# Performance work log

Measured on AMD Instinct MI355X. Metric: run time of the kernel, lower is better.

## Reference

```python
import jax, jax.numpy as jnp
import numpy as np

B, N, DIN, DOUT, H, DH, DC, NL, L = 8, 256, 64, 64, 8, 8, 64, 32, 2
SCALE = DH ** -0.5  # out_dim-per-head scaling used by both attention variants


def _ln(x, g, b):
    m = jnp.mean(x, -1, keepdims=True)
    v = jnp.mean((x - m) ** 2, -1, keepdims=True)
    return (x - m) * jax.lax.rsqrt(v + 1e-5) * g + b


def _cross_attn(x, ctx, mask_b, wq, wkv, wo, bo):
    # CrossAttentionLayer: standard softmax attention with clamp(-5,5)
    b, n, _ = x.shape
    m = ctx.shape[1]
    q = (x @ wq).reshape(b, n, H, DH).transpose(0, 2, 1, 3)
    k, v = jnp.split(ctx @ wkv, 2, axis=-1)
    k = k.reshape(b, m, H, DH).transpose(0, 2, 1, 3)
    v = v.reshape(b, m, H, DH).transpose(0, 2, 1, 3)
    sim = jnp.einsum('bhid,bhjd->bhij', q, k) * SCALE
    if mask_b is not None:
        sim = jnp.where(mask_b[:, None, None, :], sim, -jnp.finfo(sim.dtype).max)
    sim = jnp.clip(sim, -5.0, 5.0)
    attn = jax.nn.softmax(sim, axis=-1)
    out = jnp.einsum('bhij,bhjd->bhid', attn, v)
    out = out.transpose(0, 2, 1, 3).reshape(b, n, H * DH)
    return out @ wo + bo


def _mha_edge(p, e, k_RW, mask, wq, wk, we, wv):
    # GraphiT MultiHeadAttentionLayer with edge features + k_RW attention PE
    Q = (p @ wq).reshape(B, N, H, DH)
    K = (p @ wk).reshape(B, N, H, DH) * SCALE
    V = (p @ wv).reshape(B, N, H, DH).transpose(0, 2, 1, 3)  # [B,H,N,d]
    E = (e @ we).reshape(B, N, N, H, DH)
    scores = jnp.einsum('bihk,bjhk,bijhk->bhij', Q, K, E)
    scores = jnp.exp(scores - jnp.max(scores, axis=(-2, -1), keepdims=True))
    scores = scores * mask[:, None, :, None] * mask[:, None, None, :]
    scores = scores * k_RW
    denom = jnp.clip(jnp.sum(scores, -1, keepdims=True), 1e-6, None)
    out = jnp.einsum('bhij,bhjd->bhid', scores, V) / denom
    return out.transpose(0, 2, 1, 3).reshape(B, N, H * DH)


def setup_inputs() -> dict:
    key = jax.random.key(0)
    ks = jax.random.split(key, 32)
    rn = lambda k, s: jax.random.normal(k, s, dtype=jnp.float32)
    inp = {
        'h': rn(ks[0], (B, N, DIN)),
        'p': rn(ks[1], (B, N, DIN)),
        'e': rn(ks[2], (B, N, N, DIN)),
        'k_RW': jax.random.uniform(ks[3], (B, 1, N, N), dtype=jnp.float32),
        'queries': rn(ks[4], (B, NL, DC)),
        'mask': jnp.ones((B, N), dtype=jnp.float32),
        # attention_p (MultiHeadAttentionLayer) weights
        'wq_p': rn(ks[5], (DIN, H * DH)) * 0.05,
        'wk_p': rn(ks[6], (DIN, H * DH)) * 0.05,
        'we_p': rn(ks[7], (DIN, H * DH)) * 0.05,
        'wv_p': rn(ks[8], (DIN, H * DH)) * 0.05,
        'wo_p': rn(ks[9], (DOUT, DOUT)) * 0.05,
        # cross_attention_h (queries attend to nodes)
        'cq_wq': rn(ks[10], (DC, H * DH)) * 0.05,
        'cq_wkv': rn(ks[11], (DIN, 2 * H * DH)) * 0.05,
        'cq_wo': rn(ks[12], (H * DH, DC)) * 0.05,
        'cq_bo': jnp.zeros((DC,), dtype=jnp.float32),
        # L_cross latent self-attention layers (stacked)
        'sa_wq': rn(ks[13], (L, DC, H * DH)) * 0.05,
        'sa_wkv': rn(ks[14], (L, DC, 2 * H * DH)) * 0.05,
        'sa_wo': rn(ks[15], (L, H * DH, DC)) * 0.05,
        'sa_bo': jnp.zeros((L, DC), dtype=jnp.float32),
        # O_queries, norms, FFN
        'oq_w': rn(ks[16], (DC, DC)) * 0.05,
        'ln1_g': jnp.ones((DC,), dtype=jnp.float32),
        'ln1_b': jnp.zeros((DC,), dtype=jnp.float32),
        'ffn_w1': rn(ks[17], (DC, 2 * DC)) * 0.05,
        'ffn_w2': rn(ks[18], (2 * DC, DC)) * 0.05,
        'ln2_g': jnp.ones((DC,), dtype=jnp.float32),
        'ln2_b': jnp.zeros((DC,), dtype=jnp.float32),
    }
    return inp


def reference(h, p, e, k_RW, queries, mask,
              wq_p, wk_p, we_p, wv_p, wo_p,
              cq_wq, cq_wkv, cq_wo, cq_bo,
              sa_wq, sa_wkv, sa_wo, sa_bo,
              oq_w, ln1_g, ln1_b, ffn_w1, ffn_w2, ln2_g, ln2_b):
    # forward_p: update positional encoding via edge-modulated attention
    p_attn = _mha_edge(p, e, k_RW, mask, wq_p, wk_p, we_p, wv_p)
    p_new = p + jnp.tanh(p_attn @ wo_p)  # residual, no dropout (eval)
    # combine node features with updated PE (use_node_pe='sum')
    h_c = h + p_new
    mask_b = mask > 0.5
    # perceiver cross-attention: latents attend to nodes
    q = queries + _cross_attn(queries, h_c, mask_b, cq_wq, cq_wkv, cq_wo, cq_bo)
    # L_cross latent self-attention blocks with residual
    for i in range(L):
        q = q + _cross_attn(q, q, None, sa_wq[i], sa_wkv[i], sa_wo[i], sa_bo[i])
    # O_queries projection + layer norm
    q = _ln(q @ oq_w, ln1_g, ln1_b)
    # feed-forward block on queries
    ff = jax.nn.relu(q @ ffn_w1) @ ffn_w2
    q = _ln(q + ff, ln2_g, ln2_b)
    return q
```

## Files before the change

### kernel.cpp

```cpp
#include <hip/hip_runtime.h>
#include <hip/hip_bf16.h>
#include <math.h>

typedef __bf16 bf16x8 __attribute__((ext_vector_type(8)));
typedef float floatx4 __attribute__((ext_vector_type(4)));

#define ATT_SCALE 0.35355339059327373f

__device__ __forceinline__ __bf16 f2b(float x) { return (__bf16)x; }

__global__ void k_proj(const float* __restrict__ p, const float* __restrict__ quer,
                       const float* __restrict__ wq, const float* __restrict__ wk,
                       const float* __restrict__ wv, const float* __restrict__ cq_wq,
                       float* __restrict__ Q, float* __restrict__ Ks,
                       float* __restrict__ V, float* __restrict__ q1) {
  int blk = blockIdx.x, t = threadIdx.x;
  __shared__ float xr[64];
  if (blk < 2048) {
    xr[t] = p[blk * 64 + t];
    __syncthreads();
    float aq = 0.f, ak = 0.f, av = 0.f;
#pragma unroll
    for (int c = 0; c < 64; c++) {
      float x = xr[c];
      aq += x * wq[c * 64 + t];
      ak += x * wk[c * 64 + t];
      av += x * wv[c * 64 + t];
    }
    Q[blk * 64 + t] = aq;
    Ks[blk * 64 + t] = ak * ATT_SCALE;
    V[blk * 64 + t] = av;
  } else {
    int r = blk - 2048;
    xr[t] = quer[r * 64 + t];
    __syncthreads();
    float a = 0.f;
#pragma unroll
    for (int c = 0; c < 64; c++) a += xr[c] * cq_wq[c * 64 + t];
    q1[r * 64 + t] = a;
  }
}

#define LOADT(ER, JT) do {                         \
    const float* _np = ebase + (JT) * 1024;        \
    ER[0] = *(const float4*)(_np);                 \
    ER[1] = *(const float4*)(_np + 4);             \
    ER[2] = *(const float4*)(_np + 32);            \
    ER[3] = *(const float4*)(_np + 36);            \
  } while (0)

#define NTCOMP(NT, KF, VA) do {                                               \
    floatx4 acc = {0.f, 0.f, 0.f, 0.f};                                       \
    acc = __builtin_amdgcn_mfma_f32_16x16x32_bf16(wfrag[NT][0], a0, acc, 0, 0, 0); \
    acc = __builtin_amdgcn_mfma_f32_16x16x32_bf16(wfrag[NT][1], a1, acc, 0, 0, 0); \
    float s = acc[0] * KF.x * qv[NT].x + acc[1] * KF.y * qv[NT].y +           \
              acc[2] * KF.z * qv[NT].z + acc[3] * KF.w * qv[NT].w;            \
    s += __shfl_xor(s, 16);                                                   \
    float wg = __expf(s) * kwm;                                               \
    aden[NT] += wg;                                                           \
    aout[NT][0] += wg * VA.x; aout[NT][1] += wg * VA.y;                       \
    aout[NT][2] += wg * VA.z; aout[NT][3] += wg * VA.w;                       \
  } while (0)

#define STEP(JT, ER, PFSTMT) do {                                             \
    int jS = qd * 64 + (JT) * 16 + l15;                                       \
    const float* ksrow = Ks + ((long)(b * 256 + jS)) * 64 + quad * 4;         \
    const float* vrow  = V  + ((long)(b * 256 + jS)) * 64 + hsel * 8 + par * 4; \
    float4 kf0 = *(const float4*)(ksrow);                                     \
    float4 kf1 = *(const float4*)(ksrow + 16);                                \
    float4 kf2 = *(const float4*)(ksrow + 32);                                \
    float4 kf3 = *(const float4*)(ksrow + 48);                                \
    float4 va0 = *(const float4*)(vrow);                                      \
    float4 va1 = *(const float4*)(vrow + 16);                                 \
    float4 va2 = *(const float4*)(vrow + 32);                                 \
    float4 va3 = *(const float4*)(vrow + 48);                                 \
    float kwm = krw[(long)bi * 256 + jS] * mask[b * 256 + jS];                \
    __builtin_amdgcn_sched_barrier(0);                                        \
    PFSTMT;                                                                   \
    __builtin_amdgcn_sched_barrier(0);                                        \
    bf16x8 a0, a1;                                                            \
    a0[0] = f2b(ER[0].x); a0[1] = f2b(ER[0].y);                               \
    a0[2] = f2b(ER[0].z); a0[3] = f2b(ER[0].w);                               \
    a0[4] = f2b(ER[1].x); a0[5] = f2b(ER[1].y);                               \
    a0[6] = f2b(ER[1].z); a0[7] = f2b(ER[1].w);                               \
    a1[0] = f2b(ER[2].x); a1[1] = f2b(ER[2].y);                               \
    a1[2] = f2b(ER[2].z); a1[3] = f2b(ER[2].w);                               \
    a1[4] = f2b(ER[3].x); a1[5] = f2b(ER[3].y);                               \
    a1[6] = f2b(ER[3].z); a1[7] = f2b(ER[3].w);                               \
    NTCOMP(0, kf0, va0); NTCOMP(1, kf1, va1);                                 \
    NTCOMP(2, kf2, va2); NTCOMP(3, kf3, va3);                                 \
  } while (0)

__global__ __launch_bounds__(64, 1) void k_edge(
    const float* __restrict__ e, const float* __restrict__ we,
    const float* __restrict__ krw, const float* __restrict__ mask,
    const float* __restrict__ Q, const float* __restrict__ Ks,
    const float* __restrict__ V, float* __restrict__ ppart,
    float* __restrict__ pden) {
  int gid = blockIdx.x;
  int bi = gid >> 2, qd = gid & 3;
  int b = bi >> 8;
  int l = threadIdx.x;
  int l15 = l & 15, quad = l >> 4;
  int hsel = quad >> 1;
  int par = quad & 1;

  bf16x8 wfrag[4][2];
#pragma unroll
  for (int nt = 0; nt < 4; nt++)
#pragma unroll
    for (int kc = 0; kc < 2; kc++)
#pragma unroll
      for (int jj = 0; jj < 8; jj++)
        wfrag[nt][kc][jj] = f2b(we[(kc * 32 + quad * 8 + jj) * 64 + nt * 16 + l15]);

  float4 qv[4];
#pragma unroll
  for (int nt = 0; nt < 4; nt++)
    qv[nt] = *(const float4*)(Q + bi * 64 + nt * 16 + quad * 4);

  float aout[4][4];
  float aden[4] = {0.f, 0.f, 0.f, 0.f};
#pragma unroll
  for (int nt = 0; nt < 4; nt++)
#pragma unroll
    for (int d = 0; d < 4; d++) aout[nt][d] = 0.f;

  const float* ebase = e + ((long)bi * 256 + qd * 64 + l15) * 64 + quad * 8;

  float4 e0[4], e1[4], e2[4], e3[4];
  LOADT(e0, 0);
  LOADT(e1, 1);
  LOADT(e2, 2);
  __builtin_amdgcn_sched_barrier(0);

  STEP(0, e0, LOADT(e3, 3));
  STEP(1, e1, (void)0);
  STEP(2, e2, (void)0);
  STEP(3, e3, (void)0);

#pragma unroll
  for (int nt = 0; nt < 4; nt++) {
    float dn = aden[nt];
    dn += __shfl_xor(dn, 1); dn += __shfl_xor(dn, 2);
    dn += __shfl_xor(dn, 4); dn += __shfl_xor(dn, 8);
    aden[nt] = dn;
#pragma unroll
    for (int d = 0; d < 4; d++) {
      float o = aout[nt][d];
      o += __shfl_xor(o, 1); o += __shfl_xor(o, 2);
      o += __shfl_xor(o, 4); o += __shfl_xor(o, 8);
      aout[nt][d] = o;
    }
  }

  if (l15 == 0) {
#pragma unroll
    for (int nt = 0; nt < 4; nt++) {
      int head = nt * 2 + hsel;
#pragma unroll
      for (int d = 0; d < 4; d++)
        ppart[(long)gid * 64 + head * 8 + par * 4 + d] = aout[nt][d];
      if (par == 0) pden[(long)gid * 8 + head] = aden[nt];
    }
  }
}

__global__ __launch_bounds__(256) void k_post(
    const float* __restrict__ ppart, const float* __restrict__ pden,
    const float* __restrict__ mask, const float* __restrict__ hin,
    const float* __restrict__ pin, const float* __restrict__ wo,
    const float* __restrict__ cq_wkv, float* __restrict__ Kc,
    float* __restrict__ Vc) {
  int r0 = blockIdx.x * 8;
  int t = threadIdx.x;
  __shared__ float pavs[8][64];
  __shared__ float hcs[8][64];

  {
    int col = t & 63, rr = t >> 6;
#pragma unroll
    for (int k = 0; k < 2; k++) {
      int row = r0 + rr + k * 4;
      float num = 0.f, den = 0.f;
#pragma unroll
      for (int q = 0; q < 4; q++) {
        num += ppart[(long)(row * 4 + q) * 64 + col];
        den += pden[(long)(row * 4 + q) * 8 + (col >> 3)];
      }
      float mi = mask[row];
      pavs[rr + k * 4][col] = (num * mi) / fmaxf(den * mi, 1e-6f);
    }
  }
  __syncthreads();
  {
    int col = t & 63, rr = t >> 6;
    float a0 = 0.f, a1 = 0.f;
#pragma unroll
    for (int c = 0; c < 64; c++) {
      float wv = wo[c * 64 + col];
      a0 += pavs[rr][c] * wv;
      a1 += pavs[rr + 4][c] * wv;
    }
    int row0 = r0 + rr, row1 = r0 + rr + 4;
    hcs[rr][col] = hin[row0 * 64 + col] + pin[row0 * 64 + col] + tanhf(a0);
    hcs[rr + 4][col] = hin[row1 * 64 + col] + pin[row1 * 64 + col] + tanhf(a1);
  }
  __syncthreads();
  {
    int col = t & 127, rr = t >> 7;
    float a[4] = {0.f, 0.f, 0.f, 0.f};
#pragma unroll
    for (int c = 0; c < 64; c++) {
      float wv = cq_wkv[c * 128 + col];
#pragma unroll
      for (int m = 0; m < 4; m++) a[m] += hcs[rr + 2 * m][c] * wv;
    }
#pragma unroll
    for (int m = 0; m < 4; m++) {
      int row = r0 + rr + 2 * m;
      if (col < 64) Kc[row * 64 + col] = a[m];
      else          Vc[row * 64 + col - 64] = a[m];
    }
  }
}

__global__ __launch_bounds__(256) void k_crossf(
    const float* __restrict__ q1, const float* __restrict__ Kc,
    const float* __restrict__ Vc, const float* __restrict__ mask,
    const float* __restrict__ quer, const float* __restrict__ cq_wo,
    const float* __restrict__ cq_bo, const float* __restrict__ wq0,
    const float* __restrict__ wkv0, float* __restrict__ q0g,
    float* __restrict__ qqg, float* __restrict__ kvg) {
  int blk = blockIdx.x, b = blk >> 3, rg = blk & 7;
  int t = threadIdx.x, rr = t >> 6, l = t & 63, h = l >> 3, g = l & 7;
  int gr = b * 32 + rg * 4 + rr;
  __shared__ float ocs[4][64];
  __shared__ float q0s[4][64];

  {
    const float* qp = q1 + gr * 64 + h * 8;
    float4 qa = *(const float4*)qp, qb = *(const float4*)(qp + 4);
    float num[8] = {0.f, 0.f, 0.f, 0.f, 0.f, 0.f, 0.f, 0.f};
    float den = 0.f;
#pragma unroll 4
    for (int jj = 0; jj < 32; jj++) {
      int j = jj * 8 + g;
      const float* kp = Kc + (b * 256 + j) * 64 + h * 8;
      float4 ka = *(const float4*)kp, kb = *(const float4*)(kp + 4);
      float s = qa.x * ka.x + qa.y * ka.y + qa.z * ka.z + qa.w * ka.w +
                qb.x * kb.x + qb.y * kb.y + qb.z * kb.z + qb.w * kb.w;
      s *= ATT_SCALE;
      float mj = mask[b * 256 + j];
      s = (mj > 0.5f) ? s : -1e30f;
      s = fminf(fmaxf(s, -5.f), 5.f);
      float ex = __expf(s);
      den += ex;
      const float* vp = Vc + (b * 256 + j) * 64 + h * 8;
      float4 va = *(const float4*)vp, vb = *(const float4*)(vp + 4);
      num[0] += ex * va.x; num[1] += ex * va.y;
      num[2] += ex * va.z; num[3] += ex * va.w;
      num[4] += ex * vb.x; num[5] += ex * vb.y;
      num[6] += ex * vb.z; num[7] += ex * vb.w;
    }
    den += __shfl_xor(den, 1); den += __shfl_xor(den, 2); den += __shfl_xor(den, 4);
#pragma unroll
    for (int d = 0; d < 8; d++) {
      float v = num[d];
      v += __shfl_xor(v, 1); v += __shfl_xor(v, 2); v += __shfl_xor(v, 4);
      num[d] = v;
    }
    float sel = num[0];
#pragma unroll
    for (int d = 1; d < 8; d++) sel = (g == d) ? num[d] : sel;
    ocs[rr][h * 8 + g] = sel / den;
  }

  int c = l;
  {
    float acc = quer[gr * 64 + c] + cq_bo[c];
#pragma unroll
    for (int k = 0; k < 64; k++) acc += ocs[rr][k] * cq_wo[k * 64 + c];
    q0g[gr * 64 + c] = acc;
    q0s[rr][c] = acc;
  }
  {
    float aq = 0.f, ak = 0.f, av = 0.f;
#pragma unroll
    for (int k = 0; k < 64; k++) {
      float x = q0s[rr][k];
      aq += x * wq0[k * 64 + c];
      ak += x * wkv0[k * 128 + c];
      av += x * wkv0[k * 128 + 64 + c];
    }
    qqg[gr * 64 + c] = aq;
    kvg[gr * 128 + c] = ak;
    kvg[gr * 128 + 64 + c] = av;
  }
}

__global__ __launch_bounds__(256) void k_sattnf(
    const float* __restrict__ qq, const float* __restrict__ kv,
    const float* __restrict__ resid, const float* __restrict__ wo,
    const float* __restrict__ bo, const float* __restrict__ wq2,
    const float* __restrict__ wkv2, float* __restrict__ q_out,
    float* __restrict__ qq2, float* __restrict__ kv2) {
  int blk = blockIdx.x, b = blk >> 3, rg = blk & 7;
  int t = threadIdx.x, rr = t >> 6, l = t & 63, h = l >> 3, g = l & 7;
  int gr = b * 32 + rg * 4 + rr;
  __shared__ float KVs[32][128];
  __shared__ float ocs[4][64];
  __shared__ float q2s[4][64];

  const float4* s4 = (const float4*)(kv + b * 4096);
  float4* d4 = (float4*)&KVs[0][0];
#pragma unroll
  for (int i = 0; i < 4; i++) d4[i * 256 + t] = s4[i * 256 + t];

  const float* qp = qq + gr * 64 + h * 8;
  float4 qa = *(const float4*)qp, qb = *(const float4*)(qp + 4);
  __syncthreads();

  {
    float num[8] = {0.f, 0.f, 0.f, 0.f, 0.f, 0.f, 0.f, 0.f};
    float den = 0.f;
#pragma unroll
    for (int jj = 0; jj < 4; jj++) {
      int j = jj * 8 + g;
      float4 ka = *(const float4*)&KVs[j][h * 8];
      float4 kb = *(const float4*)&KVs[j][h * 8 + 4];
      float s = qa.x * ka.x + qa.y * ka.y + qa.z * ka.z + qa.w * ka.w +
                qb.x * kb.x + qb.y * kb.y + qb.z * kb.z + qb.w * kb.w;
      s *= ATT_SCALE;
      s = fminf(fmaxf(s, -5.f), 5.f);
      float ex = __expf(s);
      den += ex;
      float4 va = *(const float4*)&KVs[j][64 + h * 8];
      float4 vb = *(const float4*)&KVs[j][64 + h * 8 + 4];
      num[0] += ex * va.x; num[1] += ex * va.y;
      num[2] += ex * va.z; num[3] += ex * va.w;
      num[4] += ex * vb.x; num[5] += ex * vb.y;
      num[6] += ex * vb.z; num[7] += ex * vb.w;
    }
    den += __shfl_xor(den, 1); den += __shfl_xor(den, 2); den += __shfl_xor(den, 4);
#pragma unroll
    for (int d = 0; d < 8; d++) {
      float v = num[d];
      v += __shfl_xor(v, 1); v += __shfl_xor(v, 2); v += __shfl_xor(v, 4);
      num[d] = v;
    }
    float sel = num[0];
#pragma unroll
    for (int d = 1; d < 8; d++) sel = (g == d) ? num[d] : sel;
    ocs[rr][h * 8 + g] = sel / den;
  }

  int c = l;
  {
    float acc = resid[gr * 64 + c] + bo[c];
#pragma unroll
    for (int k = 0; k < 64; k++) acc += ocs[rr][k] * wo[k * 64 + c];
    q_out[gr * 64 + c] = acc;
    q2s[rr][c] = acc;
  }
  {
    float aq = 0.f, ak = 0.f, av = 0.f;
#pragma unroll
    for (int k = 0; k < 64; k++) {
      float x = q2s[rr][k];
      aq += x * wq2[k * 64 + c];
      ak += x * wkv2[k * 128 + c];
      av += x * wkv2[k * 128 + 64 + c];
    }
    qq2[gr * 64 + c] = aq;
    kv2[gr * 128 + c] = ak;
    kv2[gr * 128 + 64 + c] = av;
  }
}

__global__ __launch_bounds__(256) void k_finalf(
    const float* __restrict__ qq, const float* __restrict__ kv,
    const float* __restrict__ resid, const float* __restrict__ wo,
    const float* __restrict__ bo, const float* __restrict__ oqw,
    const float* __restrict__ g1, const float* __restrict__ b1,
    const float* __restrict__ w1, const float* __restrict__ w2,
    const float* __restrict__ g2, const float* __restrict__ b2v,
    float* __restrict__ out) {
  int blk = blockIdx.x, b = blk >> 3, rg = blk & 7;
  int t = threadIdx.x, rr = t >> 6, l = t & 63, h = l >> 3, g = l & 7;
  int gr = b * 32 + rg * 4 + rr;
  __shared__ float KVs[32][128];
  __shared__ float ocs[4][64];
  __shared__ float xs[4][64];
  __shared__ float hs[4][128];

  const float4* s4 = (const float4*)(kv + b * 4096);
  float4* d4 = (float4*)&KVs[0][0];
#pragma unroll
  for (int i = 0; i < 4; i++) d4[i * 256 + t] = s4[i * 256 + t];

  const float* qp = qq + gr * 64 + h * 8;
  float4 qa = *(const float4*)qp, qb = *(const float4*)(qp + 4);
  __syncthreads();

  {
    float num[8] = {0.f, 0.f, 0.f, 0.f, 0.f, 0.f, 0.f, 0.f};
    float den = 0.f;
#pragma unroll
    for (int jj = 0; jj < 4; jj++) {
      int j = jj * 8 + g;
      float4 ka = *(const float4*)&KVs[j][h * 8];
      float4 kb = *(const float4*)&KVs[j][h * 8 + 4];
      float s = qa.x * ka.x + qa.y * ka.y + qa.z * ka.z + qa.w * ka.w +
                qb.x * kb.x + qb.y * kb.y + qb.z * kb.z + qb.w * kb.w;
      s *= ATT_SCALE;
      s = fminf(fmaxf(s, -5.f), 5.f);
      float ex = __expf(s);
      den += ex;
      float4 va = *(const float4*)&KVs[j][64 + h * 8];
      float4 vb = *(const float4*)&KVs[j][64 + h * 8 + 4];
      num[0] += ex * va.x; num[1] += ex * va.y;
      num[2] += ex * va.z; num[3] += ex * va.w;
      num[4] += ex * vb.x; num[5] += ex * vb.y;
      num[6] += ex * vb.z; num[7] += ex * vb.w;
    }
    den += __shfl_xor(den, 1); den += __shfl_xor(den, 2); den += __shfl_xor(den, 4);
#pragma unroll
    for (int d = 0; d < 8; d++) {
      float v = num[d];
      v += __shfl_xor(v, 1); v += __shfl_xor(v, 2); v += __shfl_xor(v, 4);
      num[d] = v;
    }
    float sel = num[0];
#pragma unroll
    for (int d = 1; d < 8; d++) sel = (g == d) ? num[d] : sel;
    ocs[rr][h * 8 + g] = sel / den;
  }

  int c = l;
  float y;
  {
    float acc = resid[gr * 64 + c] + bo[c];
#pragma unroll
    for (int k = 0; k < 64; k++) acc += ocs[rr][k] * wo[k * 64 + c];
    xs[rr][c] = acc;
  }
  {
    float x = 0.f;
#pragma unroll
    for (int k = 0; k < 64; k++) x += xs[rr][k] * oqw[k * 64 + c];
    float m = x;
    for (int off = 1; off < 64; off <<= 1) m += __shfl_xor(m, off);
    m *= (1.f / 64.f);
    float dv = x - m, vv = dv * dv;
    for (int off = 1; off < 64; off <<= 1) vv += __shfl_xor(vv, off);
    vv *= (1.f / 64.f);
    y = dv * rsqrtf(vv + 1e-5f) * g1[c] + b1[c];
    xs[rr][c] = y;
  }
  {
    float h1 = 0.f, h2 = 0.f;
#pragma unroll
    for (int k = 0; k < 64; k++) {
      float xx = xs[rr][k];
      h1 += xx * w1[k * 128 + c];
      h2 += xx * w1[k * 128 + 64 + c];
    }
    hs[rr][c] = fmaxf(h1, 0.f);
    hs[rr][64 + c] = fmaxf(h2, 0.f);
  }
  {
    float ff = 0.f;
#pragma unroll
    for (int k = 0; k < 128; k++) ff += hs[rr][k] * w2[k * 64 + c];
    float z = y + ff;
    float m2 = z;
    for (int off = 1; off < 64; off <<= 1) m2 += __shfl_xor(m2, off);
    m2 *= (1.f / 64.f);
    float dz = z - m2, v2 = dz * dz;
    for (int off = 1; off < 64; off <<= 1) v2 += __shfl_xor(v2, off);
    v2 *= (1.f / 64.f);
    out[gr * 64 + c] = dz * rsqrtf(v2 + 1e-5f) * g2[c] + b2v[c];
  }
}

extern "C" void kernel_launch(void* const* d_in, const int* in_sizes, int n_in,
                              void* d_out, int out_size, void* d_ws, size_t ws_size,
                              hipStream_t stream) {
  const float* h_in   = (const float*)d_in[0];
  const float* p_in   = (const float*)d_in[1];
  const float* e_in   = (const float*)d_in[2];
  const float* krw    = (const float*)d_in[3];
  const float* quer   = (const float*)d_in[4];
  const float* mask   = (const float*)d_in[5];
  const float* wq_p   = (const float*)d_in[6];
  const float* wk_p   = (const float*)d_in[7];
  const float* we_p   = (const float*)d_in[8];
  const float* wv_p   = (const float*)d_in[9];
  const float* wo_p   = (const float*)d_in[10];
  const float* cq_wq  = (const float*)d_in[11];
  const float* cq_wkv = (const float*)d_in[12];
  const float* cq_wo  = (const float*)d_in[13];
  const float* cq_bo  = (const float*)d_in[14];
  const float* sa_wq  = (const float*)d_in[15];
  const float* sa_wkv = (const float*)d_in[16];
  const float* sa_wo  = (const float*)d_in[17];
  const float* sa_bo  = (const float*)d_in[18];
  const float* oq_w   = (const float*)d_in[19];
  const float* ln1_g  = (const float*)d_in[20];
  const float* ln1_b  = (const float*)d_in[21];
  const float* ffn_w1 = (const float*)d_in[22];
  const float* ffn_w2 = (const float*)d_in[23];
  const float* ln2_g  = (const float*)d_in[24];
  const float* ln2_b  = (const float*)d_in[25];

  float* ws = (float*)d_ws;
  float* Q    = ws;
  float* Ks   = Q + 131072;
  float* V    = Ks + 131072;
  float* q1   = V + 131072;
  float* Kc   = q1 + 16384;
  float* Vc   = Kc + 131072;
  float* q0   = Vc + 131072;
  float* qc1  = q0 + 16384;
  float* qqA  = qc1 + 16384;
  float* qqB  = qqA + 16384;
  float* kvA  = qqB + 16384;
  float* kvB  = kvA + 32768;
  float* ppart = kvB + 32768;
  float* pden  = ppart + 524288;

  k_proj<<<2304, 64, 0, stream>>>(p_in, quer, wq_p, wk_p, wv_p, cq_wq, Q, Ks, V, q1);
  k_edge<<<8192, 64, 0, stream>>>(e_in, we_p, krw, mask, Q, Ks, V, ppart, pden);
  k_post<<<256, 256, 0, stream>>>(ppart, pden, mask, h_in, p_in, wo_p, cq_wkv,
                                  Kc, Vc);
  k_crossf<<<64, 256, 0, stream>>>(q1, Kc, Vc, mask, quer, cq_wo, cq_bo,
                                   sa_wq, sa_wkv, q0, qqA, kvA);
  k_sattnf<<<64, 256, 0, stream>>>(qqA, kvA, q0, sa_wo, sa_bo,
                                   sa_wq + 4096, sa_wkv + 8192, qc1, qqB, kvB);
  k_finalf<<<64, 256, 0, stream>>>(qqB, kvB, qc1, sa_wo + 4096, sa_bo + 64, oq_w,
                                   ln1_g, ln1_b, ffn_w1, ffn_w2, ln2_g, ln2_b,
                                   (float*)d_out);
}
```

Measured before the change: 354.3 us.

## Stage edge tile through LDS via async global_load_lds with XOR swizzle

The 64x64 fp32 edge tile per block is now fetched with direct global-to-LDS loads into a swizzled shared buffer, replacing the register-prefetched per-step loads. All 16 loads are issued at kernel start, overlapping with weight fragment setup, then a single vmcnt wait precedes the compute steps, which read from LDS with an XOR swizzle to avoid bank conflicts. The cost is 16KB of LDS per 64-thread block and the loss of fine-grained overlap between loads and compute. There is no barrier after the wait, which relies on each lane only needing LDS writes completed by its own wave (single-wave block).

```diff
diff --git a/kernel.cpp b/kernel.cpp
--- a/kernel.cpp
+++ b/kernel.cpp
@@ -4,6 +4,8 @@
 
 typedef __bf16 bf16x8 __attribute__((ext_vector_type(8)));
 typedef float floatx4 __attribute__((ext_vector_type(4)));
+typedef __attribute__((address_space(3))) unsigned int lds_u32;
+typedef const __attribute__((address_space(1))) unsigned int glb_u32;
 
 #define ATT_SCALE 0.35355339059327373f
 
@@ -40,14 +42,6 @@
     q1[r * 64 + t] = a;
   }
 }
-
-#define LOADT(ER, JT) do {                         \
-    const float* _np = ebase + (JT) * 1024;        \
-    ER[0] = *(const float4*)(_np);                 \
-    ER[1] = *(const float4*)(_np + 4);             \
-    ER[2] = *(const float4*)(_np + 32);            \
-    ER[3] = *(const float4*)(_np + 36);            \
-  } while (0)
 
 #define NTCOMP(NT, KF, VA) do {                                               \
     floatx4 acc = {0.f, 0.f, 0.f, 0.f};                                       \
@@ -62,8 +56,14 @@
     aout[NT][2] += wg * VA.z; aout[NT][3] += wg * VA.w;                       \
   } while (0)
 
-#define STEP(JT, ER, PFSTMT) do {                                             \
-    int jS = qd * 64 + (JT) * 16 + l15;                                       \
+#define STEP9(JT) do {                                                        \
+    int r = (JT) * 16 + l15;                                                  \
+    int m = r & 15;                                                           \
+    int jS = qd * 64 + r;                                                     \
+    const float4 fA0 = *(const float4*)&elds[r * 64 + (((quad * 2 + 0) ^ m) << 2)]; \
+    const float4 fA1 = *(const float4*)&elds[r * 64 + (((quad * 2 + 1) ^ m) << 2)]; \
+    const float4 fB0 = *(const float4*)&elds[r * 64 + (((quad * 2 + 8) ^ m) << 2)]; \
+    const float4 fB1 = *(const float4*)&elds[r * 64 + (((quad * 2 + 9) ^ m) << 2)]; \
     const float* ksrow = Ks + ((long)(b * 256 + jS)) * 64 + quad * 4;         \
     const float* vrow  = V  + ((long)(b * 256 + jS)) * 64 + hsel * 8 + par * 4; \
     float4 kf0 = *(const float4*)(ksrow);                                     \
@@ -75,18 +75,11 @@
     float4 va2 = *(const float4*)(vrow + 32);                                 \
     float4 va3 = *(const float4*)(vrow + 48);                                 \
     float kwm = krw[(long)bi * 256 + jS] * mask[b * 256 + jS];                \
-    __builtin_amdgcn_sched_barrier(0);                                        \
-    PFSTMT;                                                                   \
-    __builtin_amdgcn_sched_barrier(0);                                        \
     bf16x8 a0, a1;                                                            \
-    a0[0] = f2b(ER[0].x); a0[1] = f2b(ER[0].y);                               \
-    a0[2] = f2b(ER[0].z); a0[3] = f2b(ER[0].w);                               \
-    a0[4] = f2b(ER[1].x); a0[5] = f2b(ER[1].y);                               \
-    a0[6] = f2b(ER[1].z); a0[7] = f2b(ER[1].w);                               \
-    a1[0] = f2b(ER[2].x); a1[1] = f2b(ER[2].y);                               \
-    a1[2] = f2b(ER[2].z); a1[3] = f2b(ER[2].w);                               \
-    a1[4] = f2b(ER[3].x); a1[5] = f2b(ER[3].y);                               \
-    a1[6] = f2b(ER[3].z); a1[7] = f2b(ER[3].w);                               \
+    a0[0] = f2b(fA0.x); a0[1] = f2b(fA0.y); a0[2] = f2b(fA0.z); a0[3] = f2b(fA0.w); \
+    a0[4] = f2b(fA1.x); a0[5] = f2b(fA1.y); a0[6] = f2b(fA1.z); a0[7] = f2b(fA1.w); \
+    a1[0] = f2b(fB0.x); a1[1] = f2b(fB0.y); a1[2] = f2b(fB0.z); a1[3] = f2b(fB0.w); \
+    a1[4] = f2b(fB1.x); a1[5] = f2b(fB1.y); a1[6] = f2b(fB1.z); a1[7] = f2b(fB1.w); \
     NTCOMP(0, kf0, va0); NTCOMP(1, kf1, va1);                                 \
     NTCOMP(2, kf2, va2); NTCOMP(3, kf3, va3);                                 \
   } while (0)
@@ -105,6 +98,20 @@
   int hsel = quad >> 1;
   int par = quad & 1;
 
+  __shared__ __align__(16) float elds[64 * 64];
+
+  {
+    const float* ebb = e + (long)(bi * 256 + qd * 64) * 64;
+#pragma unroll
+    for (int k = 0; k < 16; k++) {
+      int L = k * 64 + l;
+      int row = L >> 4, g = L & 15;
+      const float* src = ebb + row * 64 + ((g ^ (row & 15)) << 2);
+      __builtin_amdgcn_global_load_lds((glb_u32*)src, (lds_u32*)&elds[k * 256],
+                                       16, 0, 0);
+    }
+  }
+
   bf16x8 wfrag[4][2];
 #pragma unroll
   for (int nt = 0; nt < 4; nt++)
@@ -126,18 +133,14 @@
 #pragma unroll
     for (int d = 0; d < 4; d++) aout[nt][d] = 0.f;
 
-  const float* ebase = e + ((long)bi * 256 + qd * 64 + l15) * 64 + quad * 8;
-
-  float4 e0[4], e1[4], e2[4], e3[4];
-  LOADT(e0, 0);
-  LOADT(e1, 1);
-  LOADT(e2, 2);
   __builtin_amdgcn_sched_barrier(0);
-
-  STEP(0, e0, LOADT(e3, 3));
-  STEP(1, e1, (void)0);
-  STEP(2, e2, (void)0);
-  STEP(3, e3, (void)0);
+  asm volatile("s_waitcnt vmcnt(0)" ::: "memory");
+  __builtin_amdgcn_sched_barrier(0);
+
+  STEP9(0);
+  STEP9(1);
+  STEP9(2);
+  STEP9(3);
 
 #pragma unroll
   for (int nt = 0; nt < 4; nt++) {
```

Measured after the change: 358.1 us. No clear change (+1.1%).
